# Kernel optimization log

Hardware: AMD Instinct MI355X
Metric: run time of the kernel (lower is better)

## Reference

```python
import jax, jax.numpy as jnp
import numpy as np

NUM_HEADS = 16


def setup_inputs() -> dict:
    key = jax.random.key(0)
    ks = jax.random.split(key, 8)
    b, n, m, L, d = 2, 1024, 4, 1024, 1024
    x = jax.random.normal(ks[0], (b, n, d), dtype=jnp.float32)
    context = jax.random.normal(ks[1], (b, m, L, d), dtype=jnp.float32)
    doc_similarities = jax.random.normal(ks[2], (b, m), dtype=jnp.float32)
    mask = jnp.ones((b, n), dtype=bool)
    context_mask = jnp.ones((b, m, L), dtype=bool)
    Wq = jax.random.normal(ks[3], (d, d), dtype=jnp.float32) * 0.02
    Wkv = jax.random.normal(ks[4], (d, 2 * d), dtype=jnp.float32) * 0.02
    Wout = jax.random.normal(ks[5], (d, d), dtype=jnp.float32) * 0.02
    bout = jnp.zeros((d,), dtype=jnp.float32)
    beta = jnp.ones((), dtype=jnp.float32)
    return {"x": x, "context": context, "doc_similarities": doc_similarities,
            "mask": mask, "context_mask": context_mask,
            "Wq": Wq, "Wkv": Wkv, "Wout": Wout, "bout": bout, "beta": beta}


def reference(x, context, doc_similarities, mask, context_mask, Wq, Wkv, Wout, bout, beta):
    b, n, d = x.shape
    h = NUM_HEADS
    hd = d // h
    _, m, L, _ = context.shape
    kv_len = m * L

    # q projection -> (b, h, n, hd)
    q = (x @ Wq).reshape(b, n, h, hd).transpose(0, 2, 1, 3)

    ctx = context.reshape(b, kv_len, d)
    cmask = context_mask.reshape(b, kv_len)

    # doc similarity bias, broadcast per-token within each doc, scaled by beta
    ds = jnp.repeat(doc_similarities[:, :, None], L, axis=-1).reshape(b, kv_len)
    ds = ds[:, None, None, :] * beta  # (b, 1, 1, kv_len)

    kv = ctx @ Wkv  # (b, kv_len, 2d)
    k, v = jnp.split(kv, 2, axis=-1)
    k = k.reshape(b, kv_len, h, hd).transpose(0, 2, 3, 1)  # (b, h, hd, kv_len)
    v = v.reshape(b, kv_len, h, hd).transpose(0, 2, 1, 3)  # (b, h, kv_len, hd)

    # NOTE: original scales by d**-0.5 (full model dim), not head_size**-0.5
    attention_pre_doc_sim = (q @ k) * (d ** -0.5)  # (b, h, n, kv_len)
    attention = attention_pre_doc_sim + ds

    # faithful mask path: multiply by cross mask, then map exact zeros to -inf
    cross_mask = mask[:, None, :, None] * cmask[:, None, None, :]  # (b,1,n,kv_len)
    attention = attention * cross_mask
    attention = jnp.where(attention == 0.0, -jnp.inf, attention)

    attention_weights = jax.nn.softmax(attention, axis=-1)
    # dropout_rate = 0.0 -> identity

    out = (attention_weights @ v).transpose(0, 2, 1, 3).reshape(b, n, d)
    out = out @ Wout + bout
    return out, attention_pre_doc_sim
```

## Files before the change

kernel.cpp:

```cpp
#include <hip/hip_runtime.h>
#include <cstdint>
#include <cstddef>

typedef unsigned short u16t;
typedef __attribute__((ext_vector_type(4))) float f32x4;
typedef __attribute__((ext_vector_type(4))) int i32x4;
typedef __attribute__((ext_vector_type(4))) unsigned int u32x4;
typedef __attribute__((ext_vector_type(8))) __bf16 bf16x8;
typedef __attribute__((ext_vector_type(4))) __bf16 bf16x4;
typedef __attribute__((ext_vector_type(8))) unsigned short u16x8;
typedef __attribute__((ext_vector_type(4))) unsigned short u16x4;

#define INFF __builtin_inff()

__device__ __forceinline__ u16t f2b(float f) {
  union { float f; unsigned u; } x; x.f = f;
  unsigned r = x.u + 0x7FFFu + ((x.u >> 16) & 1u);
  return (u16t)(r >> 16);
}

__device__ __forceinline__ void gload16(const u16t* g, u16t* l) {
  __builtin_amdgcn_global_load_lds((const __attribute__((address_space(1))) void*)g,
                                   (__attribute__((address_space(3))) void*)l, 16, 0, 0);
}

__global__ __launch_bounds__(256) void k_prep(const float* __restrict__ x,
                                              const float* __restrict__ ctx,
                                              u16t* __restrict__ x16,
                                              u16t* __restrict__ ctx16,
                                              const int* __restrict__ cmask,
                                              unsigned int* __restrict__ cmbits) {
  const int bx = blockIdx.x, tid = threadIdx.x;
  if (bx < 2048) {
    int i = bx * 256 + tid;
    f32x4 v = *(const f32x4*)(x + (size_t)i * 4);
    u16x4 o;
    o[0] = f2b(v[0]); o[1] = f2b(v[1]); o[2] = f2b(v[2]); o[3] = f2b(v[3]);
    *(u16x4*)(x16 + (size_t)i * 4) = o;
  } else if (bx < 10240) {
    int i = (bx - 2048) * 256 + tid;
    f32x4 v = *(const f32x4*)(ctx + (size_t)i * 4);
    u16x4 o;
    o[0] = f2b(v[0]); o[1] = f2b(v[1]); o[2] = f2b(v[2]); o[3] = f2b(v[3]);
    *(u16x4*)(ctx16 + (size_t)i * 4) = o;
  } else {
    int b = tid >> 7, wdi = tid & 127;
    const int* cp = cmask + b * 4096 + wdi * 32;
    unsigned int bits = 0;
#pragma unroll
    for (int i = 0; i < 32; ++i) bits |= (cp[i] != 0 ? 1u : 0u) << i;
    cmbits[tid] = bits;
  }
}

__global__ __launch_bounds__(256) void k_transpose_w3(const float* __restrict__ Wq,
                                                      const float* __restrict__ Wkv,
                                                      const float* __restrict__ Wout,
                                                      u16t* __restrict__ WqT,
                                                      u16t* __restrict__ WkvT,
                                                      u16t* __restrict__ WoutT) {
  __shared__ float tile[64 * 65];
  const int t = threadIdx.x;
  const int bxx = blockIdx.x;
  const float* src; u16t* dst; int C, cb;
  if (bxx < 16)      { src = Wq;   dst = WqT;   C = 1024; cb = bxx * 64; }
  else if (bxx < 48) { src = Wkv;  dst = WkvT;  C = 2048; cb = (bxx - 16) * 64; }
  else               { src = Wout; dst = WoutT; C = 1024; cb = (bxx - 48) * 64; }
  const int rb = blockIdx.y * 64;
#pragma unroll
  for (int it = 0; it < 4; ++it) {
    int c = it * 256 + t;
    int r = c >> 4, ch = c & 15;
    f32x4 v = *(const f32x4*)(src + (size_t)(rb + r) * C + cb + ch * 4);
    float* dp = &tile[r * 65 + ch * 4];
    dp[0] = v[0]; dp[1] = v[1]; dp[2] = v[2]; dp[3] = v[3];
  }
  __syncthreads();
#pragma unroll
  for (int it = 0; it < 2; ++it) {
    int c = it * 256 + t;
    int dr = c >> 3, ch = c & 7;
    u16x8 o;
#pragma unroll
    for (int i = 0; i < 8; ++i) o[i] = f2b(tile[(ch * 8 + i) * 65 + dr]);
    *(u16x8*)(dst + (size_t)(cb + dr) * 1024 + rb + ch * 8) = o;
  }
}

template <int MODE>
__global__ __launch_bounds__(256) void k_gemm_bt(const u16t* __restrict__ A,
                                                 const u16t* __restrict__ Bt,
                                                 void* __restrict__ C,
                                                 u16t* __restrict__ C2,
                                                 const float* __restrict__ bias,
                                                 float oscale,
                                                 int K, int lda, int ldb, int ldc, int nbx) {
  __shared__ u16t As[128 * 64];
  __shared__ u16t Bs[128 * 64];
  const int tid = threadIdx.x;
  const int lane = tid & 63, wid = tid >> 6;
  const int l16 = lane & 15, lg = lane >> 4;
  const int wr = wid >> 1, wc = wid & 1;
  const int g = blockIdx.x, per = gridDim.x >> 3;
  const int w = (g & 7) * per + (g >> 3);
  const int bx = w % nbx, by = w / nbx;
  const int brow = by * 128, bcol = bx * 128;
  const int sr = lane >> 3, chs = lane & 7;
  f32x4 acc[4][4] = {};

  for (int k0 = 0; k0 < K; k0 += 64) {
#pragma unroll
    for (int it = 0; it < 4; ++it) {
      int row = it * 32 + wid * 8 + sr;
      int ch = chs ^ (row & 7);
      gload16(A + (size_t)(brow + row) * lda + k0 + ch * 8, &As[it * 2048 + wid * 512]);
      gload16(Bt + (size_t)(bcol + row) * ldb + k0 + ch * 8, &Bs[it * 2048 + wid * 512]);
    }
    __syncthreads();
#pragma unroll
    for (int kk = 0; kk < 2; ++kk) {
      bf16x8 af[4], bfv[4];
#pragma unroll
      for (int mi = 0; mi < 4; ++mi) {
        int row = wr * 64 + mi * 16 + l16;
        int kch = (kk * 4 + lg) ^ (row & 7);
        af[mi] = *(const bf16x8*)(&As[row * 64 + kch * 8]);
      }
#pragma unroll
      for (int ni = 0; ni < 4; ++ni) {
        int row = wc * 64 + ni * 16 + l16;
        int kch = (kk * 4 + lg) ^ (row & 7);
        bfv[ni] = *(const bf16x8*)(&Bs[row * 64 + kch * 8]);
      }
#pragma unroll
      for (int mi = 0; mi < 4; ++mi)
#pragma unroll
        for (int ni = 0; ni < 4; ++ni)
          acc[mi][ni] = __builtin_amdgcn_mfma_f32_16x16x32_bf16(af[mi], bfv[ni], acc[mi][ni], 0, 0, 0);
    }
    __syncthreads();
  }

  if (MODE == 2 && bcol >= 1024) {
#pragma unroll
    for (int mi = 0; mi < 4; ++mi) {
#pragma unroll
      for (int ni = 0; ni < 4; ++ni) {
        int vcol = bcol - 1024 + wc * 64 + ni * 16 + l16;
        int h = vcol >> 6, hd = vcol & 63;
        int row0 = brow + wr * 64 + mi * 16 + lg * 4;
        int bb = row0 >> 12, pos = row0 & 4095;
        u16x4 o4;
#pragma unroll
        for (int j = 0; j < 4; ++j) o4[j] = f2b(acc[mi][ni][j]);
        *(u16x4*)(C2 + ((size_t)((bb * 16 + h) * 64 + hd)) * 4096 + pos) = o4;
      }
    }
    return;
  }
#pragma unroll
  for (int mi = 0; mi < 4; ++mi) {
#pragma unroll
    for (int ni = 0; ni < 4; ++ni) {
#pragma unroll
      for (int j = 0; j < 4; ++j) {
        size_t row = (size_t)brow + wr * 64 + mi * 16 + lg * 4 + j;
        int col = bcol + wc * 64 + ni * 16 + l16;
        float v = acc[mi][ni][j] * oscale;
        if (MODE == 1) {
          v += bias[col];
          __builtin_nontemporal_store(v, (float*)C + row * ldc + col);
        } else {
          ((u16t*)C)[row * ldc + col] = f2b(v);
        }
      }
    }
  }
}

__global__ __launch_bounds__(256) void k_attn(const u16t* __restrict__ k16,
                                              const u16t* __restrict__ vT16,
                                              const u16t* __restrict__ q16,
                                              const unsigned int* __restrict__ cmbits,
                                              const float* __restrict__ dsim,
                                              const float* __restrict__ beta_p,
                                              const int* __restrict__ mask,
                                              float* __restrict__ pre,
                                              u16t* __restrict__ O16) {
  __shared__ u16t Ks[128 * 64];
  __shared__ u16t Vs[64 * 128];
  __shared__ u16t Ps[4 * 2048];
  __shared__ float Sf[4 * 2048];

  const int tid = threadIdx.x;
  const int lane = tid & 63, wid = tid >> 6;
  const int l16 = lane & 15, lg = lane >> 4;
  const int g = blockIdx.x;
  const int w = (g & 7) * 64 + (g >> 3);
  const int nb = w & 15, hb = w >> 4;
  const int h = hb & 15, b = hb >> 4;
  const int qrow0 = nb * 64 + wid * 16;

  bf16x8 aq0, aq1;
  {
    const u16t* qp = q16 + (size_t)(b * 1024 + qrow0 + l16) * 1024 + h * 64 + lg * 8;
    aq0 = *(const bf16x8*)(qp);
    aq1 = *(const bf16x8*)(qp + 32);
  }
  const bool qm = mask[b * 1024 + qrow0 + l16] != 0;

  const float beta = beta_p[0];
  const float ds40 = dsim[b * 4 + 0] * beta, ds41 = dsim[b * 4 + 1] * beta;
  const float ds42 = dsim[b * 4 + 2] * beta, ds43 = dsim[b * 4 + 3] * beta;

  float mrow = -INFF, lsum = 0.f;
  f32x4 o[4] = {};

  const u16t* kbase = k16 + (size_t)b * 4096 * 1024 + (size_t)h * 64;
  const u16t* vbase = vT16 + (size_t)(b * 16 + h) * 64 * 4096;
  float* preb = pre + (size_t)((b * 16 + h) * 1024 + qrow0) * 4096;
  const u32x4* cmw = (const u32x4*)(cmbits + b * 128);
  char* Pwb = (char*)&Ps[wid * 2048] + l16 * 256;
  const int pswz = (l16 & 7) << 4;
  char* Swave = (char*)&Sf[wid * 2048];
  char* Swb = Swave + l16 * 512;

  auto stage = [&](int kv0s) {
    u16t* Kb = &Ks[wid * 2048];
    u16t* Vb = &Vs[wid * 2048];
#pragma unroll
    for (int it = 0; it < 4; ++it) {
      int row = wid * 32 + it * 8 + (lane >> 3);
      int ch = (lane & 7) ^ (row & 7);
      gload16(kbase + (size_t)(kv0s + row) * 1024 + ch * 8, Kb + it * 512);
    }
#pragma unroll
    for (int it = 0; it < 4; ++it) {
      int row = wid * 16 + it * 4 + (lane >> 4);
      int ch = (lane & 15) ^ (row & 7);
      gload16(vbase + (size_t)row * 4096 + kv0s + ch * 8, Vb + it * 512);
    }
  };

  auto storepass = [&](int kv0p) {
    const int rhalf = lane >> 5, c4 = (lane & 31) * 4;
#pragma unroll
    for (int i = 0; i < 8; ++i) {
      const int row2 = i * 2 + rhalf;
      f32x4 v = *(const f32x4*)(Swave + row2 * 512 + ((c4 * 4) ^ ((row2 & 7) << 4)));
      __builtin_nontemporal_store(v, (f32x4*)(preb + (size_t)row2 * 4096 + kv0p + c4));
    }
  };

  for (int t = 0; t < 32; ++t) {
    const u32x4 Wc = cmw[t];
    stage(t * 128);
    asm volatile("" ::: "memory");
    if (t > 0) storepass((t - 1) * 128);
    if (t == 0) {
      asm volatile("s_waitcnt vmcnt(0) lgkmcnt(0)" ::: "memory");
    } else {
      asm volatile("s_waitcnt vmcnt(8) lgkmcnt(0)" ::: "memory");
    }
    __builtin_amdgcn_sched_barrier(0);
    __builtin_amdgcn_s_barrier();
    __builtin_amdgcn_sched_barrier(0);

    const int kv0 = t * 128;
    const int d = t >> 3;
    const float ds_t = (d & 1) ? ((d & 2) ? ds43 : ds41) : ((d & 2) ? ds42 : ds40);

    f32x4 s[8];
#pragma unroll
    for (int kb = 0; kb < 8; ++kb) {
      f32x4 acc = {0.f, 0.f, 0.f, 0.f};
      int row = kb * 16 + l16;
      bf16x8 bk0 = *(const bf16x8*)(&Ks[row * 64 + ((lg ^ (row & 7)) << 3)]);
      bf16x8 bk1 = *(const bf16x8*)(&Ks[row * 64 + (((4 + lg) ^ (row & 7)) << 3)]);
      acc = __builtin_amdgcn_mfma_f32_16x16x32_bf16(bk0, aq0, acc, 0, 0, 0);
      acc = __builtin_amdgcn_mfma_f32_16x16x32_bf16(bk1, aq1, acc, 0, 0, 0);
      s[kb] = acc;
    }

    float tmax = -INFF;
#pragma unroll
    for (int kb = 0; kb < 8; ++kb) {
      *(f32x4*)(Swb + ((kb * 64 + lg * 16) ^ pswz)) = s[kb];
      const unsigned int sh = Wc[kb >> 1] >> ((kb & 1) * 16 + lg * 4);
#pragma unroll
      for (int j = 0; j < 4; ++j) {
        float bias = ((sh >> j) & 1u) ? ds_t : -INFF;
        float t2 = s[kb][j] + bias;
        if (!qm) t2 = 0.f;
        if (t2 == 0.f) t2 = -INFF;
        s[kb][j] = t2;
        tmax = fmaxf(tmax, t2);
      }
    }
    tmax = fmaxf(tmax, __shfl_xor(tmax, 16, 64));
    tmax = fmaxf(tmax, __shfl_xor(tmax, 32, 64));
    const float mold = mrow;
    const float mn = fmaxf(mold, tmax);
    const bool nochange = __all(mn == mold);
    mrow = mn;

    float psum = 0.f;
#pragma unroll
    for (int kb = 0; kb < 8; ++kb) {
      bf16x4 pb;
#pragma unroll
      for (int j = 0; j < 4; ++j) {
        float p = (mn == -INFF) ? 0.f : __expf(s[kb][j] - mn);
        psum += p;
        pb[j] = (__bf16)p;
      }
      *(bf16x4*)(Pwb + ((kb * 32 + lg * 8) ^ pswz)) = pb;
    }
    asm volatile("" ::: "memory");
    psum += __shfl_xor(psum, 16, 64);
    psum += __shfl_xor(psum, 32, 64);

    if (nochange) {
      lsum += psum;
    } else {
      const float fs = (mn == -INFF) ? 0.f : __expf(mold - mn);
      lsum = lsum * fs + psum;
      float fsj[4];
#pragma unroll
      for (int j = 0; j < 4; ++j) fsj[j] = __shfl(fs, lg * 4 + j, 64);
#pragma unroll
      for (int ni = 0; ni < 4; ++ni)
#pragma unroll
        for (int j = 0; j < 4; ++j) o[ni][j] *= fsj[j];
    }

#pragma unroll
    for (int kk2 = 0; kk2 < 4; ++kk2) {
      bf16x8 pa = *(const bf16x8*)(Pwb + ((kk2 * 64 + lg * 16) ^ pswz));
#pragma unroll
      for (int ni = 0; ni < 4; ++ni) {
        int vrow = ni * 16 + l16;
        bf16x8 vb = *(const bf16x8*)(&Vs[vrow * 128 + (((kk2 * 4 + lg) ^ (vrow & 7)) << 3)]);
        o[ni] = __builtin_amdgcn_mfma_f32_16x16x32_bf16(pa, vb, o[ni], 0, 0, 0);
      }
    }

    asm volatile("s_waitcnt lgkmcnt(0)" ::: "memory");
    __builtin_amdgcn_sched_barrier(0);
    __builtin_amdgcn_s_barrier();
    __builtin_amdgcn_sched_barrier(0);
  }
  storepass(31 * 128);

  float lsj[4];
#pragma unroll
  for (int j = 0; j < 4; ++j) lsj[j] = __shfl(lsum, lg * 4 + j, 64);
#pragma unroll
  for (int ni = 0; ni < 4; ++ni) {
#pragma unroll
    for (int j = 0; j < 4; ++j) {
      size_t row = (size_t)b * 1024 + qrow0 + lg * 4 + j;
      int col = h * 64 + ni * 16 + l16;
      O16[row * 1024 + col] = f2b(o[ni][j] / lsj[j]);
    }
  }
}

extern "C" void kernel_launch(void* const* d_in, const int* in_sizes, int n_in,
                              void* d_out, int out_size, void* d_ws, size_t ws_size,
                              hipStream_t stream) {
  const float* x = (const float*)d_in[0];
  const float* ctx = (const float*)d_in[1];
  const float* dsim = (const float*)d_in[2];
  const int* mask = (const int*)d_in[3];
  const int* cmask = (const int*)d_in[4];
  const float* Wq = (const float*)d_in[5];
  const float* Wkv = (const float*)d_in[6];
  const float* Wout = (const float*)d_in[7];
  const float* bout = (const float*)d_in[8];
  const float* beta = (const float*)d_in[9];

  char* ws = (char*)d_ws;
  u16t* q16 = (u16t*)(ws + (0ull << 20));
  u16t* k16 = (u16t*)(ws + (4ull << 20));
  u16t* vT16 = (u16t*)(ws + (36ull << 20));
  u16t* O16 = (u16t*)(ws + (52ull << 20));
  u16t* x16 = (u16t*)(ws + (56ull << 20));
  u16t* ctx16 = (u16t*)(ws + (60ull << 20));
  u16t* WqT = (u16t*)(ws + (76ull << 20));
  u16t* WkvT = (u16t*)(ws + (78ull << 20));
  u16t* WoutT = (u16t*)(ws + (82ull << 20));
  unsigned int* cmbits = (unsigned int*)(ws + (84ull << 20));

  float* outp = (float*)d_out;
  float* pre = outp + (size_t)2 * 1024 * 1024;

  k_prep<<<10241, 256, 0, stream>>>(x, ctx, x16, ctx16, cmask, cmbits);
  k_transpose_w3<<<dim3(64, 16), 256, 0, stream>>>(Wq, Wkv, Wout, WqT, WkvT, WoutT);

  k_gemm_bt<0><<<128, 256, 0, stream>>>(x16, WqT, (void*)q16, nullptr, nullptr, 0.03125f, 1024, 1024, 1024, 1024, 8);
  k_gemm_bt<2><<<1024, 256, 0, stream>>>(ctx16, WkvT, (void*)k16, vT16, nullptr, 1.0f, 1024, 1024, 1024, 1024, 16);
  k_attn<<<512, 256, 0, stream>>>(k16, vT16, q16, cmbits, dsim, beta, mask, pre, O16);
  k_gemm_bt<1><<<128, 256, 0, stream>>>(O16, WoutT, d_out, nullptr, bout, 1.0f, 1024, 1024, 1024, 1024, 8);
}
```

Measured before the change: 224.7 us.

## Merge prep/transpose and Q/KV GEMM launches; stage V-transpose stores through LDS

Folds the weight-transpose work into the prep kernel and the Q and KV projection GEMMs into one launch, cutting kernel launches and filling the GPU better for the small Q GEMM. The V-transposed epilogue now writes through a swizzled LDS tile so each global store is a 16-byte contiguous write instead of scattered 8-byte stores. This adds two extra block barriers in the epilogue and a larger prep kernel in which blocks take different paths.

```diff
diff --git a/kernel.cpp b/kernel.cpp
--- a/kernel.cpp
+++ b/kernel.cpp
@@ -4,7 +4,6 @@
 
 typedef unsigned short u16t;
 typedef __attribute__((ext_vector_type(4))) float f32x4;
-typedef __attribute__((ext_vector_type(4))) int i32x4;
 typedef __attribute__((ext_vector_type(4))) unsigned int u32x4;
 typedef __attribute__((ext_vector_type(8))) __bf16 bf16x8;
 typedef __attribute__((ext_vector_type(4))) __bf16 bf16x4;
@@ -29,7 +28,13 @@
                                               u16t* __restrict__ x16,
                                               u16t* __restrict__ ctx16,
                                               const int* __restrict__ cmask,
-                                              unsigned int* __restrict__ cmbits) {
+                                              unsigned int* __restrict__ cmbits,
+                                              const float* __restrict__ Wq,
+                                              const float* __restrict__ Wkv,
+                                              const float* __restrict__ Wout,
+                                              u16t* __restrict__ WqT,
+                                              u16t* __restrict__ WkvT,
+                                              u16t* __restrict__ WoutT) {
   const int bx = blockIdx.x, tid = threadIdx.x;
   if (bx < 2048) {
     int i = bx * 256 + tid;
@@ -37,39 +42,34 @@
     u16x4 o;
     o[0] = f2b(v[0]); o[1] = f2b(v[1]); o[2] = f2b(v[2]); o[3] = f2b(v[3]);
     *(u16x4*)(x16 + (size_t)i * 4) = o;
+    return;
   } else if (bx < 10240) {
     int i = (bx - 2048) * 256 + tid;
     f32x4 v = *(const f32x4*)(ctx + (size_t)i * 4);
     u16x4 o;
     o[0] = f2b(v[0]); o[1] = f2b(v[1]); o[2] = f2b(v[2]); o[3] = f2b(v[3]);
     *(u16x4*)(ctx16 + (size_t)i * 4) = o;
-  } else {
+    return;
+  } else if (bx == 10240) {
     int b = tid >> 7, wdi = tid & 127;
     const int* cp = cmask + b * 4096 + wdi * 32;
     unsigned int bits = 0;
 #pragma unroll
     for (int i = 0; i < 32; ++i) bits |= (cp[i] != 0 ? 1u : 0u) << i;
     cmbits[tid] = bits;
-  }
-}
-
-__global__ __launch_bounds__(256) void k_transpose_w3(const float* __restrict__ Wq,
-                                                      const float* __restrict__ Wkv,
-                                                      const float* __restrict__ Wout,
-                                                      u16t* __restrict__ WqT,
-                                                      u16t* __restrict__ WkvT,
-                                                      u16t* __restrict__ WoutT) {
+    return;
+  }
   __shared__ float tile[64 * 65];
-  const int t = threadIdx.x;
-  const int bxx = blockIdx.x;
+  const int id = bx - 10241;
+  const int bxx = id & 63;
   const float* src; u16t* dst; int C, cb;
   if (bxx < 16)      { src = Wq;   dst = WqT;   C = 1024; cb = bxx * 64; }
   else if (bxx < 48) { src = Wkv;  dst = WkvT;  C = 2048; cb = (bxx - 16) * 64; }
   else               { src = Wout; dst = WoutT; C = 1024; cb = (bxx - 48) * 64; }
-  const int rb = blockIdx.y * 64;
+  const int rb = (id >> 6) * 64;
 #pragma unroll
   for (int it = 0; it < 4; ++it) {
-    int c = it * 256 + t;
+    int c = it * 256 + tid;
     int r = c >> 4, ch = c & 15;
     f32x4 v = *(const f32x4*)(src + (size_t)(rb + r) * C + cb + ch * 4);
     float* dp = &tile[r * 65 + ch * 4];
@@ -78,7 +78,7 @@
   __syncthreads();
 #pragma unroll
   for (int it = 0; it < 2; ++it) {
-    int c = it * 256 + t;
+    int c = it * 256 + tid;
     int dr = c >> 3, ch = c & 7;
     u16x8 o;
 #pragma unroll
@@ -88,20 +88,19 @@
 }
 
 template <int MODE>
-__global__ __launch_bounds__(256) void k_gemm_bt(const u16t* __restrict__ A,
-                                                 const u16t* __restrict__ Bt,
-                                                 void* __restrict__ C,
-                                                 u16t* __restrict__ C2,
-                                                 const float* __restrict__ bias,
-                                                 float oscale,
-                                                 int K, int lda, int ldb, int ldc, int nbx) {
-  __shared__ u16t As[128 * 64];
-  __shared__ u16t Bs[128 * 64];
+__device__ __forceinline__ void gemm_body(int g, int per, int nbx,
+                                          const u16t* __restrict__ A,
+                                          const u16t* __restrict__ Bt,
+                                          void* __restrict__ C,
+                                          u16t* __restrict__ C2,
+                                          const float* __restrict__ bias,
+                                          float oscale,
+                                          int K, int lda, int ldb, int ldc,
+                                          u16t* As, u16t* Bs) {
   const int tid = threadIdx.x;
   const int lane = tid & 63, wid = tid >> 6;
   const int l16 = lane & 15, lg = lane >> 4;
   const int wr = wid >> 1, wc = wid & 1;
-  const int g = blockIdx.x, per = gridDim.x >> 3;
   const int w = (g & 7) * per + (g >> 3);
   const int bx = w % nbx, by = w / nbx;
   const int brow = by * 128, bcol = bx * 128;
@@ -142,20 +141,31 @@
   }
 
   if (MODE == 2 && bcol >= 1024) {
-#pragma unroll
-    for (int mi = 0; mi < 4; ++mi) {
-#pragma unroll
-      for (int ni = 0; ni < 4; ++ni) {
-        int vcol = bcol - 1024 + wc * 64 + ni * 16 + l16;
-        int h = vcol >> 6, hd = vcol & 63;
-        int row0 = brow + wr * 64 + mi * 16 + lg * 4;
-        int bb = row0 >> 12, pos = row0 & 4095;
-        u16x4 o4;
-#pragma unroll
-        for (int j = 0; j < 4; ++j) o4[j] = f2b(acc[mi][ni][j]);
-        *(u16x4*)(C2 + ((size_t)((bb * 16 + h) * 64 + hd)) * 4096 + pos) = o4;
-      }
-    }
+    u16t* L = As;
+#pragma unroll
+    for (int ni = 0; ni < 4; ++ni) {
+      int vcol = wc * 64 + ni * 16 + l16;
+      int swz = (vcol & 7) << 4;
+#pragma unroll
+      for (int mi = 0; mi < 4; ++mi) {
+        int pos0 = wr * 64 + mi * 16 + lg * 4;
+        u16x4 pb;
+#pragma unroll
+        for (int j = 0; j < 4; ++j) pb[j] = f2b(acc[mi][ni][j]);
+        *(u16x4*)((char*)L + vcol * 256 + ((pos0 * 2) ^ swz)) = pb;
+      }
+    }
+    __syncthreads();
+    const int bb = brow >> 12, basepos = brow & 4095;
+#pragma unroll
+    for (int p = 0; p < 8; ++p) {
+      int o = p * 4096 + tid * 16;
+      int r = o >> 8, bix = o & 255;
+      u16x8 v = *(const u16x8*)((char*)L + r * 256 + (bix ^ ((r & 7) << 4)));
+      int gv = bcol - 1024 + r, h = gv >> 6, hd = gv & 63;
+      *(u16x8*)(C2 + ((size_t)((bb * 16 + h) * 64 + hd)) * 4096 + basepos + (bix >> 1)) = v;
+    }
+    __syncthreads();
     return;
   }
 #pragma unroll
@@ -176,6 +186,33 @@
       }
     }
   }
+}
+
+__global__ __launch_bounds__(256) void k_gemm_qkv(const u16t* __restrict__ x16,
+                                                  const u16t* __restrict__ WqT,
+                                                  u16t* __restrict__ q16,
+                                                  const u16t* __restrict__ ctx16,
+                                                  const u16t* __restrict__ WkvT,
+                                                  u16t* __restrict__ k16,
+                                                  u16t* __restrict__ vT16) {
+  __shared__ u16t smem[2 * 128 * 64];
+  u16t* As = smem;
+  u16t* Bs = smem + 128 * 64;
+  if (blockIdx.x < 1024)
+    gemm_body<2>(blockIdx.x, 128, 16, ctx16, WkvT, (void*)k16, vT16, nullptr, 1.0f,
+                 1024, 1024, 1024, 1024, As, Bs);
+  else
+    gemm_body<0>(blockIdx.x - 1024, 16, 8, x16, WqT, (void*)q16, nullptr, nullptr, 0.03125f,
+                 1024, 1024, 1024, 1024, As, Bs);
+}
+
+__global__ __launch_bounds__(256) void k_gemm_out(const u16t* __restrict__ O16,
+                                                  const u16t* __restrict__ WoutT,
+                                                  float* __restrict__ out,
+                                                  const float* __restrict__ bout) {
+  __shared__ u16t smem[2 * 128 * 64];
+  gemm_body<1>(blockIdx.x, 16, 8, O16, WoutT, (void*)out, nullptr, bout, 1.0f,
+               1024, 1024, 1024, 1024, smem, smem + 128 * 64);
 }
 
 __global__ __launch_bounds__(256) void k_attn(const u16t* __restrict__ k16,
@@ -395,11 +432,9 @@
   float* outp = (float*)d_out;
   float* pre = outp + (size_t)2 * 1024 * 1024;
 
-  k_prep<<<10241, 256, 0, stream>>>(x, ctx, x16, ctx16, cmask, cmbits);
-  k_transpose_w3<<<dim3(64, 16), 256, 0, stream>>>(Wq, Wkv, Wout, WqT, WkvT, WoutT);
-
-  k_gemm_bt<0><<<128, 256, 0, stream>>>(x16, WqT, (void*)q16, nullptr, nullptr, 0.03125f, 1024, 1024, 1024, 1024, 8);
-  k_gemm_bt<2><<<1024, 256, 0, stream>>>(ctx16, WkvT, (void*)k16, vT16, nullptr, 1.0f, 1024, 1024, 1024, 1024, 16);
+  k_prep<<<11265, 256, 0, stream>>>(x, ctx, x16, ctx16, cmask, cmbits,
+                                    Wq, Wkv, Wout, WqT, WkvT, WoutT);
+  k_gemm_qkv<<<1152, 256, 0, stream>>>(x16, WqT, q16, ctx16, WkvT, k16, vT16);
   k_attn<<<512, 256, 0, stream>>>(k16, vT16, q16, cmbits, dsim, beta, mask, pre, O16);
-  k_gemm_bt<1><<<128, 256, 0, stream>>>(O16, WoutT, d_out, nullptr, bout, 1.0f, 1024, 1024, 1024, 1024, 8);
-}
+  k_gemm_out<<<128, 256, 0, stream>>>(O16, WoutT, (float*)d_out, bout);
+}
```

Result: faster. 214.5 us (median of 5 runs) (-4.5%).
